# Kernel optimization log

Hardware: AMD Instinct MI355X
Metric: run time of the kernel (lower is better)

The kernel has to match this reference:

```python
import jax, jax.numpy as jnp
import numpy as np

N_NODES = 50000
N_EDGES = 500000
N_GRAPHS = 2000
HID = 145
N_CLS = 21
N_LAYERS = 4
EPS = 1e-5

def setup_inputs() -> dict:
    key = jax.random.key(0)
    ks = jax.random.split(key, 12)
    x = jax.random.randint(ks[0], (N_NODES,), 0, N_CLS)
    edge_index = jax.random.randint(ks[1], (2, N_EDGES), 0, N_NODES)
    batch_idx = jnp.sort(jax.random.randint(ks[2], (N_NODES,), 0, N_GRAPHS))
    s = 1.0 / np.sqrt(HID)
    emb = jax.random.normal(ks[3], (N_CLS, HID), jnp.float32)
    Wc = jax.random.uniform(ks[4], (N_LAYERS, HID, HID), jnp.float32, -s, s)
    bc = jax.random.uniform(ks[5], (N_LAYERS, HID), jnp.float32, -s, s)
    gamma = jnp.ones((N_LAYERS, HID), jnp.float32)
    beta = jnp.zeros((N_LAYERS, HID), jnp.float32)
    W1 = jax.random.uniform(ks[6], (HID, HID // 2), jnp.float32, -s, s)
    b1 = jax.random.uniform(ks[7], (HID // 2,), jnp.float32, -s, s)
    W2 = jax.random.uniform(ks[8], (HID // 2, 1), jnp.float32, -s, s)
    b2 = jax.random.uniform(ks[9], (1,), jnp.float32, -s, s)
    return {"x": x, "edge_index": edge_index, "batch_idx": batch_idx,
            "emb": emb, "Wc": Wc, "bc": bc, "gamma": gamma, "beta": beta,
            "W1": W1, "b1": b1, "W2": W2, "b2": b2}

def reference(x, edge_index, batch_idx, emb, Wc, bc, gamma, beta, W1, b1, W2, b2):
    N = x.shape[0]
    # gcn_norm with self loops: deg over targets (col), sym normalization
    loops = jnp.arange(N)
    row = jnp.concatenate([edge_index[0], loops])  # source
    col = jnp.concatenate([edge_index[1], loops])  # target
    deg = jax.ops.segment_sum(jnp.ones_like(row, jnp.float32), col, num_segments=N)
    dis = jnp.where(deg > 0, jax.lax.rsqrt(deg), 0.0)
    ew = dis[row] * dis[col]  # [E+N]

    h = emb[x]  # [N, HID]
    for l in range(N_LAYERS):
        h_in = h
        hw = h @ Wc[l]                                   # linear
        msg = hw[row] * ew[:, None]                      # gather + weight
        agg = jax.ops.segment_sum(msg, col, num_segments=N) + bc[l]  # scatter-add
        # BatchNorm1d (training-mode batch stats, biased var)
        mu = jnp.mean(agg, axis=0)
        var = jnp.mean((agg - mu) ** 2, axis=0)
        hbn = gamma[l] * (agg - mu) * jax.lax.rsqrt(var + EPS) + beta[l]
        h = jax.nn.relu(hbn) + h_in                      # relu + residual
    # global mean pool
    sums = jax.ops.segment_sum(h, batch_idx, num_segments=N_GRAPHS)
    cnt = jax.ops.segment_sum(jnp.ones((N,), jnp.float32), batch_idx, num_segments=N_GRAPHS)
    hg = sums / jnp.maximum(cnt, 1.0)[:, None]
    out = jax.nn.relu(hg @ W1 + b1) @ W2 + b2
    return out.reshape(-1, 1)
```

## Files before the change

### kernel.cpp

```cpp
#include <hip/hip_runtime.h>

#define N_NODES  50000
#define N_EDGES  500000
#define N_GRAPHS 2000
#define HID      145
#define HID2     72
#define N_LAYERS 4
#define EPS      1e-5f
#define HWS_LD   160
#define AGG_LD   152
#define BR       64
#define TSB      168
#define NBKT     64
#define GPSZ     (NBKT * 2 * AGG_LD)
#define NB_FILL  ((N_EDGES + 255) / 256)

typedef __attribute__((ext_vector_type(4))) float f32x4;
typedef __attribute__((ext_vector_type(2))) _Float16 f16x2;
typedef __attribute__((ext_vector_type(8))) _Float16 f16x8;

#define RFL(v) __builtin_amdgcn_readfirstlane(v)


__global__ void k_zero(int* __restrict__ hist, float* __restrict__ gpart) {
    int i = blockIdx.x * 256 + threadIdx.x;
    if (i < N_NODES) hist[i] = 0;
    if (i < N_LAYERS * GPSZ) gpart[i] = 0.f;
}


__global__ void k_hist(const int* __restrict__ col, int* __restrict__ hist) {
    int i = blockIdx.x * 256 + threadIdx.x;
    if (i < N_EDGES) atomicAdd(&hist[col[i]], 1);
}

__global__ void k_scan1(const int* __restrict__ cnt, int* __restrict__ incl,
                        int* __restrict__ part) {
    __shared__ int s[1024];
    int i = blockIdx.x * 1024 + threadIdx.x;
    int v = (i < N_NODES) ? cnt[i] : 0;
    s[threadIdx.x] = v;
    __syncthreads();
    for (int d = 1; d < 1024; d <<= 1) {
        int t = (threadIdx.x >= d) ? s[threadIdx.x - d] : 0;
        __syncthreads();
        s[threadIdx.x] += t;
        __syncthreads();
    }
    if (i < N_NODES) incl[i] = s[threadIdx.x];
    if (threadIdx.x == 1023) part[blockIdx.x] = s[1023];
}


__global__ void k_scan3(const int* __restrict__ incl, const int* __restrict__ cnt,
                        const int* __restrict__ part, int* __restrict__ starts,
                        int* __restrict__ cursor, float* __restrict__ dis) {
    __shared__ int sOff;
    int t = threadIdx.x;
    if (t < 64) {
        int v = (t < (int)blockIdx.x && t < 49) ? part[t] : 0;
#pragma unroll
        for (int d = 32; d > 0; d >>= 1) v += __shfl_xor(v, d);
        if (t == 0) sOff = v;
    }
    __syncthreads();
    int off = sOff;
    int i = blockIdx.x * 1024 + t;
    if (i < N_NODES) {
        int st = incl[i] - cnt[i] + off;
        starts[i] = st;
        cursor[i] = st;
        dis[i] = rsqrtf((float)(cnt[i] + 1));
    }
    if (i == 0) starts[N_NODES] = N_EDGES;
}


__global__ void k_fill_wfrag(const int* __restrict__ rowv, const int* __restrict__ colv,
                             int* __restrict__ cursor, int* __restrict__ csr,
                             const float* __restrict__ Wc, _Float16* __restrict__ Wfrag) {
    int b = blockIdx.x;
    if (b < NB_FILL) {
        int e = b * 256 + threadIdx.x;
        if (e < N_EDGES) {
            int c = colv[e];
            int p = atomicAdd(&cursor[c], 1);
            csr[p] = rowv[e];
        }
    } else {
        int fid = (b - NB_FILL) * 4 + (threadIdx.x >> 6);
        int l = threadIdx.x & 63;
        int layer = fid / 50, rem = fid - layer * 50;
        int kc = rem / 10, ct = rem - kc * 10;
        const float* Wl = Wc + (size_t)layer * HID * HID;
        _Float16* base = Wfrag + (size_t)fid * 512 + l * 8;
#pragma unroll
        for (int j = 0; j < 8; j++) {
            int k = kc * 32 + (l >> 4) * 8 + j;
            int c = ct * 16 + (l & 15);
            float v = (k < HID && c < HID) ? Wl[k * HID + c] : 0.f;
            base[j] = (_Float16)v;
        }
    }
}


#define MFMA16(a, b, c) __builtin_amdgcn_mfma_f32_16x16x32_f16(a, b, c, 0, 0, 0)

template <int MODE>
__global__ __launch_bounds__(512, 6) void k_gemm_fused(
    const _Float16* __restrict__ wfb, const float* __restrict__ dis,
    const int* __restrict__ x, const float* __restrict__ emb,
    const _Float16* __restrict__ agg, const float* __restrict__ gpart,
    const float* __restrict__ gamma, const float* __restrict__ beta,
    _Float16* __restrict__ h, _Float16* __restrict__ hws) {
    __shared__ _Float16 tile[BR * TSB];
    __shared__ float sA[HID], sB[HID];
    int t = threadIdx.x;
    int rbase = blockIdx.x * BR;
    if (MODE == 1 && t < HID) {
        float s_ = 0.f, q_ = 0.f;
        for (int b = 0; b < NBKT; b++) {
            s_ += gpart[b * (2 * AGG_LD) + t];
            q_ += gpart[b * (2 * AGG_LD) + AGG_LD + t];
        }
        const float inv = 1.f / (float)N_NODES;
        float mu = s_ * inv;
        float var = q_ * inv - mu * mu;
        float a = gamma[t] * rsqrtf(var + EPS);
        sA[t] = a;
        sB[t] = beta[t] - mu * a;
    }
    __syncthreads();
    for (int idx = t; idx < BR * 19; idx += 512) {
        int r = idx / 19;
        int c = idx - r * 19;
        int f0 = c * 8;
        int gr = rbase + r;
        f16x8 hst = {};
        if (gr < N_NODES) {
            size_t base = (size_t)gr * AGG_LD + f0;
            if (MODE == 0) {
                const float* er = emb + x[gr] * HID;
#pragma unroll
                for (int j = 0; j < 8; j++) {
                    int f = f0 + j;
                    hst[j] = (_Float16)((f < HID) ? er[f] : 0.f);
                }
            } else {
                f16x8 av = *(const f16x8*)(agg + base);
                f16x8 hv = *(const f16x8*)(h + base);
#pragma unroll
                for (int j = 0; j < 8; j++) {
                    int f = f0 + j;
                    float vj = 0.f;
                    if (f < HID) {
                        vj = fmaf(sA[f], (float)av[j], sB[f]);
                        vj = fmaxf(vj, 0.f) + (float)hv[j];
                    }
                    hst[j] = (_Float16)vj;
                }
            }
            *(f16x8*)(h + base) = hst;
        }
        *(f16x8*)&tile[r * TSB + f0] = hst;
    }
    if (t < BR) {
        f16x8 z = {};
        *(f16x8*)&tile[t * TSB + 152] = z;
    }
    __syncthreads();

    int w = t >> 6, l = t & 63;
    int rt = w & 3;
    int c5 = (w >> 2) * 5;
    int arow = rt * 16 + (l & 15);
    int kgrp = (l >> 4) * 8;
    f32x4 acc0 = {}, acc1 = {}, acc2 = {}, acc3 = {}, acc4 = {};
#pragma unroll
    for (int kc = 0; kc < 5; kc++) {
        f16x8 ah = *(const f16x8*)&tile[arow * TSB + kc * 32 + kgrp];
        const _Float16* p = wfb + (size_t)(kc * 10 + c5) * 512 + l * 8;
        f16x8 bh;
#define STEP(ACC, CI)                                                      \
        bh = *(const f16x8*)(p + (CI) * 512);                              \
        ACC = MFMA16(ah, bh, ACC);
        STEP(acc0, 0) STEP(acc1, 1) STEP(acc2, 2) STEP(acc3, 3) STEP(acc4, 4)
#undef STEP
    }
    int rb4 = rbase + rt * 16 + (l >> 4) * 4;
    f32x4 d4 = *(const f32x4*)(dis + rb4);
    int colb = c5 * 16 + (l & 15);
#pragma unroll
    for (int r_ = 0; r_ < 4; r_++) {
        int gr = rb4 + r_;
        if (gr < N_NODES) {
            float dd = d4[r_];
            _Float16* row = hws + (size_t)gr * HWS_LD + colb;
            row[0]  = (_Float16)(acc0[r_] * dd);
            row[16] = (_Float16)(acc1[r_] * dd);
            row[32] = (_Float16)(acc2[r_] * dd);
            row[48] = (_Float16)(acc3[r_] * dd);
            row[64] = (_Float16)(acc4[r_] * dd);
        }
    }
}


__global__ __launch_bounds__(256) void k_agg(const _Float16* __restrict__ hws,
                                             const int* __restrict__ starts,
                                             const int* __restrict__ csr,
                                             const float* __restrict__ dis,
                                             _Float16* __restrict__ agg,
                                             float* __restrict__ gpart) {
    __shared__ float sS[4][AGG_LD], sQ[4][AGG_LD];
    int t = threadIdx.x;
    int wave = t >> 6;
    int lane = t & 63;
    int i = RFL(blockIdx.x * 4 + wave);
    int s = RFL(starts[i]);
    int e = RFL(starts[i + 1]);
    bool tl = lane < 9;
    const f16x2* self = (const f16x2*)(hws + (size_t)i * HWS_LD);
    f16x2 sv = self[lane];
    float ax = (float)sv.x, ay = (float)sv.y;
    float bx = 0.f, by = 0.f;
    if (tl) { f16x2 tv = self[64 + lane]; bx = (float)tv.x; by = (float)tv.y; }
    int last = e - 1;
    for (int j = s; j < e; j += 8) {
        int rb[8]; float m[8];
#pragma unroll
        for (int u = 0; u < 8; u++) {
            int jj = j + u;
            bool ok = jj < e;
            rb[u] = RFL(csr[ok ? jj : last]) * HWS_LD;
            m[u] = ok ? 1.f : 0.f;
        }
#pragma unroll
        for (int u = 0; u < 8; u++) {
            f16x2 v = ((const f16x2*)(hws + rb[u]))[lane];
            ax = fmaf((float)v.x, m[u], ax);
            ay = fmaf((float)v.y, m[u], ay);
        }
        if (tl) {
#pragma unroll
            for (int u = 0; u < 8; u++) {
                f16x2 v = ((const f16x2*)(hws + rb[u]))[64 + lane];
                bx = fmaf((float)v.x, m[u], bx);
                by = fmaf((float)v.y, m[u], by);
            }
        }
    }
    float di = dis[i];
    float v0 = ax * di, v1 = ay * di;
    float v2 = bx * di;
    float v3 = (lane < 8) ? by * di : 0.f;

    f16x2* o2 = (f16x2*)(agg + (size_t)i * AGG_LD);
    o2[lane] = f16x2{(_Float16)v0, (_Float16)v1};
    if (tl) o2[64 + lane] = f16x2{(_Float16)v2, (_Float16)v3};

    sS[wave][2 * lane] = v0;     sQ[wave][2 * lane] = v0 * v0;
    sS[wave][2 * lane + 1] = v1; sQ[wave][2 * lane + 1] = v1 * v1;
    if (tl) {
        sS[wave][128 + 2 * lane] = v2; sQ[wave][128 + 2 * lane] = v2 * v2;
        sS[wave][129 + 2 * lane] = v3; sQ[wave][129 + 2 * lane] = v3 * v3;
    }
    __syncthreads();
    int bucket = blockIdx.x & (NBKT - 1);
    float* gp = gpart + (size_t)bucket * (2 * AGG_LD);
    for (int idx2 = t; idx2 < 2 * AGG_LD; idx2 += 256) {
        int f = (idx2 < AGG_LD) ? idx2 : idx2 - AGG_LD;
        if (f > HID) continue;
        float v = (idx2 < AGG_LD)
                      ? ((sS[0][f] + sS[1][f]) + (sS[2][f] + sS[3][f]))
                      : ((sQ[0][f] + sQ[1][f]) + (sQ[2][f] + sQ[3][f]));
        atomicAdd(&gp[idx2], v);
    }
}


__global__ __launch_bounds__(256) void k_bncoef(const float* __restrict__ gpart,
                                                const float* __restrict__ gamma,
                                                const float* __restrict__ beta,
                                                float* __restrict__ AB) {
    int w = blockIdx.x * 4 + (threadIdx.x >> 6);
    int lane = threadIdx.x & 63;
    if (w >= HID) return;
    const float* ps = gpart + (size_t)lane * (2 * AGG_LD) + w;
    float s = ps[0];
    float q = ps[AGG_LD];
#pragma unroll
    for (int d = 32; d > 0; d >>= 1) {
        s += __shfl_xor(s, d);
        q += __shfl_xor(q, d);
    }
    if (lane == 0) {
        const float inv = 1.f / (float)N_NODES;
        float mu = s * inv;
        float var = q * inv - mu * mu;
        float a = gamma[w] * rsqrtf(var + EPS);
        AB[w] = a;
        AB[HID + w] = beta[w] - mu * a;
    }
}


__global__ __launch_bounds__(192) void k_pool_mlp(
    const _Float16* __restrict__ agg, const _Float16* __restrict__ h,
    const float* __restrict__ AB, const int* __restrict__ batch,
    const float* __restrict__ W1, const float* __restrict__ b1,
    const float* __restrict__ W2, const float* __restrict__ b2,
    float* __restrict__ out) {
    __shared__ float sH[HID];
    __shared__ float red[128];
    int g = blockIdx.x;
    int lo = 0, hi = N_NODES;
    while (lo < hi) { int m = (lo + hi) >> 1; if (batch[m] < g) lo = m + 1; else hi = m; }
    int s = lo;
    hi = N_NODES;
    while (lo < hi) { int m = (lo + hi) >> 1; if (batch[m] < g + 1) lo = m + 1; else hi = m; }
    int e = lo;
    int f = threadIdx.x;
    if (f < HID) {
        float A = AB[f], B = AB[HID + f];
        float acc = 0.f;
        for (int n = s; n < e; n++) {
            size_t idx = (size_t)n * AGG_LD + f;
            float v = fmaf(A, (float)agg[idx], B);
            acc += fmaxf(v, 0.f) + (float)h[idx];
        }
        sH[f] = acc / fmaxf((float)(e - s), 1.f);
    }
    __syncthreads();
    int t = threadIdx.x;
    float v = 0.f;
    if (t < HID2) {
        float acc = b1[t];
        for (int k = 0; k < HID; k++) acc = fmaf(sH[k], W1[k * HID2 + t], acc);
        v = fmaxf(acc, 0.f) * W2[t];
    }
    if (t < 128) red[t] = v;
    __syncthreads();
    for (int d = 64; d > 0; d >>= 1) {
        if (t < d) red[t] += red[t + d];
        __syncthreads();
    }
    if (t == 0) out[g] = red[0] + b2[0];
}


extern "C" void kernel_launch(void* const* d_in, const int* in_sizes, int n_in,
                              void* d_out, int out_size, void* d_ws, size_t ws_size,
                              hipStream_t stream) {
    const int*   x     = (const int*)d_in[0];
    const int*   erow  = (const int*)d_in[1];
    const int*   ecol  = erow + N_EDGES;
    const int*   batch = (const int*)d_in[2];
    const float* emb   = (const float*)d_in[3];
    const float* Wc    = (const float*)d_in[4];
    const float* gamma = (const float*)d_in[6];
    const float* beta  = (const float*)d_in[7];
    const float* W1    = (const float*)d_in[8];
    const float* b1    = (const float*)d_in[9];
    const float* W2    = (const float*)d_in[10];
    const float* b2    = (const float*)d_in[11];
    float* out = (float*)d_out;

    char* wsb = (char*)d_ws;
    size_t off = 0;
    auto alloc = [&](size_t bytes) -> char* {
        char* p = wsb + off;
        off = (off + bytes + 255) & ~(size_t)255;
        return p;
    };
    int*      hist    = (int*)alloc(N_NODES * 4);
    int*      incl    = (int*)alloc(N_NODES * 4);
    int*      part    = (int*)alloc(64 * 4);
    int*      starts  = (int*)alloc((N_NODES + 1) * 4);
    int*      cursor  = (int*)alloc(N_NODES * 4);
    int*      csr     = (int*)alloc(N_EDGES * 4);
    float*    dis     = (float*)alloc((N_NODES + 64) * 4);
    _Float16* h       = (_Float16*)alloc((size_t)N_NODES * AGG_LD * 2);
    _Float16* hws     = (_Float16*)alloc((size_t)N_NODES * HWS_LD * 2);
    _Float16* agg     = (_Float16*)alloc((size_t)N_NODES * AGG_LD * 2);
    float*    gpart   = (float*)alloc((size_t)N_LAYERS * GPSZ * 4);
    float*    AB      = (float*)alloc(2 * HID * 4);
    _Float16* Wfrag   = (_Float16*)alloc((size_t)N_LAYERS * 50 * 512 * 2);

    const int NB_SCAN = (N_NODES + 1023) / 1024;
    const int NB_GEMM = (N_NODES + BR - 1) / BR;
    const int NB_ZERO = (N_LAYERS * GPSZ + 255) / 256;

    k_zero<<<(N_NODES > N_LAYERS * GPSZ ? (N_NODES + 255) / 256 : NB_ZERO), 256, 0, stream>>>(hist, gpart);
    k_hist<<<(N_EDGES + 255) / 256, 256, 0, stream>>>(ecol, hist);
    k_scan1<<<NB_SCAN, 1024, 0, stream>>>(hist, incl, part);
    k_scan3<<<NB_SCAN, 1024, 0, stream>>>(incl, hist, part, starts, cursor, dis);
    k_fill_wfrag<<<NB_FILL + 50, 256, 0, stream>>>(erow, ecol, cursor, csr, Wc, Wfrag);

    for (int l = 0; l < N_LAYERS; l++) {
        const _Float16* wfb = Wfrag + (size_t)l * 50 * 512;
        if (l == 0)
            k_gemm_fused<0><<<NB_GEMM, 512, 0, stream>>>(
                wfb, dis, x, emb, agg, nullptr, nullptr, nullptr, h, hws);
        else
            k_gemm_fused<1><<<NB_GEMM, 512, 0, stream>>>(
                wfb, dis, x, emb, agg, gpart + (size_t)(l - 1) * GPSZ,
                gamma + (l - 1) * HID, beta + (l - 1) * HID, h, hws);
        k_agg<<<N_NODES / 4, 256, 0, stream>>>(hws, starts, csr, dis, agg,
                                               gpart + (size_t)l * GPSZ);
    }

    k_bncoef<<<(HID + 3) / 4, 256, 0, stream>>>(gpart + (size_t)3 * GPSZ,
                                                gamma + 3 * HID, beta + 3 * HID, AB);
    k_pool_mlp<<<N_GRAPHS, 192, 0, stream>>>(agg, h, AB, batch, W1, b1, W2, b2, out);
}
```

Measured before the change: 381.6 us.

## Merge scan kernels, fold BN coef into pool, split agg loop, halve buckets

Merges the two-pass prefix scan into one kernel in which each block recomputes its own offset by summing the preceding counts. The final-layer BN coefficient kernel is folded into the pooling kernel, so every block recomputes the coefficients from the bucket partials. The aggregation loop gets a mask-free main loop over full groups of eight edges and a masked tail, and the number of stats buckets drops from 64 to 32. The intent is fewer kernel launches and less work in the inner loop, at the cost of redundant reads in the scan and pool kernels and more atomic contention per bucket.

```diff
diff --git a/kernel.cpp b/kernel.cpp
--- a/kernel.cpp
+++ b/kernel.cpp
@@ -11,7 +11,7 @@
 #define AGG_LD   152
 #define BR       64
 #define TSB      168
-#define NBKT     64
+#define NBKT     32
 #define GPSZ     (NBKT * 2 * AGG_LD)
 #define NB_FILL  ((N_EDGES + 255) / 256)
 
@@ -34,43 +34,39 @@
     if (i < N_EDGES) atomicAdd(&hist[col[i]], 1);
 }
 
-__global__ void k_scan1(const int* __restrict__ cnt, int* __restrict__ incl,
-                        int* __restrict__ part) {
+
+__global__ void k_scan(const int* __restrict__ cnt, int* __restrict__ starts,
+                       int* __restrict__ cursor, float* __restrict__ dis) {
     __shared__ int s[1024];
-    int i = blockIdx.x * 1024 + threadIdx.x;
+    __shared__ int sOff;
+    int b = blockIdx.x, t = threadIdx.x;
+    int i = b * 1024 + t;
     int v = (i < N_NODES) ? cnt[i] : 0;
-    s[threadIdx.x] = v;
+    int pre = 0;
+    for (int k = t; k < b * 1024; k += 1024) pre += cnt[k];
+    s[t] = pre;
+    __syncthreads();
+    for (int d = 512; d > 0; d >>= 1) {
+        if (t < d) s[t] += s[t + d];
+        __syncthreads();
+    }
+    if (t == 0) sOff = s[0];
+    __syncthreads();
+    int off = sOff;
+    __syncthreads();
+    s[t] = v;
     __syncthreads();
     for (int d = 1; d < 1024; d <<= 1) {
-        int t = (threadIdx.x >= d) ? s[threadIdx.x - d] : 0;
+        int x = (t >= d) ? s[t - d] : 0;
         __syncthreads();
-        s[threadIdx.x] += t;
+        s[t] += x;
         __syncthreads();
     }
-    if (i < N_NODES) incl[i] = s[threadIdx.x];
-    if (threadIdx.x == 1023) part[blockIdx.x] = s[1023];
-}
-
-
-__global__ void k_scan3(const int* __restrict__ incl, const int* __restrict__ cnt,
-                        const int* __restrict__ part, int* __restrict__ starts,
-                        int* __restrict__ cursor, float* __restrict__ dis) {
-    __shared__ int sOff;
-    int t = threadIdx.x;
-    if (t < 64) {
-        int v = (t < (int)blockIdx.x && t < 49) ? part[t] : 0;
-#pragma unroll
-        for (int d = 32; d > 0; d >>= 1) v += __shfl_xor(v, d);
-        if (t == 0) sOff = v;
-    }
-    __syncthreads();
-    int off = sOff;
-    int i = blockIdx.x * 1024 + t;
     if (i < N_NODES) {
-        int st = incl[i] - cnt[i] + off;
+        int st = off + s[t] - v;
         starts[i] = st;
         cursor[i] = st;
-        dis[i] = rsqrtf((float)(cnt[i] + 1));
+        dis[i] = rsqrtf((float)(v + 1));
     }
     if (i == 0) starts[N_NODES] = N_EDGES;
 }
@@ -226,14 +222,36 @@
     float ax = (float)sv.x, ay = (float)sv.y;
     float bx = 0.f, by = 0.f;
     if (tl) { f16x2 tv = self[64 + lane]; bx = (float)tv.x; by = (float)tv.y; }
-    int last = e - 1;
-    for (int j = s; j < e; j += 8) {
+
+    int nfull = (e - s) & ~7;
+    int efull = s + nfull;
+    int j = s;
+    for (; j < efull; j += 8) {
+        int rb[8];
+#pragma unroll
+        for (int u = 0; u < 8; u++) rb[u] = RFL(csr[j + u]) * HWS_LD;
+#pragma unroll
+        for (int u = 0; u < 8; u++) {
+            f16x2 v = ((const f16x2*)(hws + rb[u]))[lane];
+            ax += (float)v.x;
+            ay += (float)v.y;
+        }
+        if (tl) {
+#pragma unroll
+            for (int u = 0; u < 8; u++) {
+                f16x2 v = ((const f16x2*)(hws + rb[u]))[64 + lane];
+                bx += (float)v.x;
+                by += (float)v.y;
+            }
+        }
+    }
+    if (j < e) {
+        int last = e - 1;
         int rb[8]; float m[8];
 #pragma unroll
         for (int u = 0; u < 8; u++) {
-            int jj = j + u;
-            bool ok = jj < e;
-            rb[u] = RFL(csr[ok ? jj : last]) * HWS_LD;
+            bool ok = j + u < e;
+            rb[u] = RFL(csr[ok ? j + u : last]) * HWS_LD;
             m[u] = ok ? 1.f : 0.f;
         }
 #pragma unroll
@@ -251,6 +269,7 @@
             }
         }
     }
+
     float di = dis[i];
     float v0 = ax * di, v1 = ay * di;
     float v2 = bx * di;
@@ -280,40 +299,31 @@
 }
 
 
-__global__ __launch_bounds__(256) void k_bncoef(const float* __restrict__ gpart,
-                                                const float* __restrict__ gamma,
-                                                const float* __restrict__ beta,
-                                                float* __restrict__ AB) {
-    int w = blockIdx.x * 4 + (threadIdx.x >> 6);
-    int lane = threadIdx.x & 63;
-    if (w >= HID) return;
-    const float* ps = gpart + (size_t)lane * (2 * AGG_LD) + w;
-    float s = ps[0];
-    float q = ps[AGG_LD];
-#pragma unroll
-    for (int d = 32; d > 0; d >>= 1) {
-        s += __shfl_xor(s, d);
-        q += __shfl_xor(q, d);
-    }
-    if (lane == 0) {
-        const float inv = 1.f / (float)N_NODES;
-        float mu = s * inv;
-        float var = q * inv - mu * mu;
-        float a = gamma[w] * rsqrtf(var + EPS);
-        AB[w] = a;
-        AB[HID + w] = beta[w] - mu * a;
-    }
-}
-
-
 __global__ __launch_bounds__(192) void k_pool_mlp(
     const _Float16* __restrict__ agg, const _Float16* __restrict__ h,
-    const float* __restrict__ AB, const int* __restrict__ batch,
+    const float* __restrict__ gpart, const float* __restrict__ gamma,
+    const float* __restrict__ beta, const int* __restrict__ batch,
     const float* __restrict__ W1, const float* __restrict__ b1,
     const float* __restrict__ W2, const float* __restrict__ b2,
     float* __restrict__ out) {
+    __shared__ float sA[HID], sB[HID];
     __shared__ float sH[HID];
     __shared__ float red[128];
+    int f = threadIdx.x;
+    if (f < HID) {
+        float s_ = 0.f, q_ = 0.f;
+        for (int b = 0; b < NBKT; b++) {
+            s_ += gpart[b * (2 * AGG_LD) + f];
+            q_ += gpart[b * (2 * AGG_LD) + AGG_LD + f];
+        }
+        const float inv = 1.f / (float)N_NODES;
+        float mu = s_ * inv;
+        float var = q_ * inv - mu * mu;
+        float a = gamma[f] * rsqrtf(var + EPS);
+        sA[f] = a;
+        sB[f] = beta[f] - mu * a;
+    }
+    __syncthreads();
     int g = blockIdx.x;
     int lo = 0, hi = N_NODES;
     while (lo < hi) { int m = (lo + hi) >> 1; if (batch[m] < g) lo = m + 1; else hi = m; }
@@ -321,9 +331,8 @@
     hi = N_NODES;
     while (lo < hi) { int m = (lo + hi) >> 1; if (batch[m] < g + 1) lo = m + 1; else hi = m; }
     int e = lo;
-    int f = threadIdx.x;
     if (f < HID) {
-        float A = AB[f], B = AB[HID + f];
+        float A = sA[f], B = sB[f];
         float acc = 0.f;
         for (int n = s; n < e; n++) {
             size_t idx = (size_t)n * AGG_LD + f;
@@ -375,8 +384,6 @@
         return p;
     };
     int*      hist    = (int*)alloc(N_NODES * 4);
-    int*      incl    = (int*)alloc(N_NODES * 4);
-    int*      part    = (int*)alloc(64 * 4);
     int*      starts  = (int*)alloc((N_NODES + 1) * 4);
     int*      cursor  = (int*)alloc(N_NODES * 4);
     int*      csr     = (int*)alloc(N_EDGES * 4);
@@ -385,17 +392,14 @@
     _Float16* hws     = (_Float16*)alloc((size_t)N_NODES * HWS_LD * 2);
     _Float16* agg     = (_Float16*)alloc((size_t)N_NODES * AGG_LD * 2);
     float*    gpart   = (float*)alloc((size_t)N_LAYERS * GPSZ * 4);
-    float*    AB      = (float*)alloc(2 * HID * 4);
     _Float16* Wfrag   = (_Float16*)alloc((size_t)N_LAYERS * 50 * 512 * 2);
 
     const int NB_SCAN = (N_NODES + 1023) / 1024;
     const int NB_GEMM = (N_NODES + BR - 1) / BR;
-    const int NB_ZERO = (N_LAYERS * GPSZ + 255) / 256;
-
-    k_zero<<<(N_NODES > N_LAYERS * GPSZ ? (N_NODES + 255) / 256 : NB_ZERO), 256, 0, stream>>>(hist, gpart);
+
+    k_zero<<<(N_NODES + 255) / 256, 256, 0, stream>>>(hist, gpart);
     k_hist<<<(N_EDGES + 255) / 256, 256, 0, stream>>>(ecol, hist);
-    k_scan1<<<NB_SCAN, 1024, 0, stream>>>(hist, incl, part);
-    k_scan3<<<NB_SCAN, 1024, 0, stream>>>(incl, hist, part, starts, cursor, dis);
+    k_scan<<<NB_SCAN, 1024, 0, stream>>>(hist, starts, cursor, dis);
     k_fill_wfrag<<<NB_FILL + 50, 256, 0, stream>>>(erow, ecol, cursor, csr, Wc, Wfrag);
 
     for (int l = 0; l < N_LAYERS; l++) {
@@ -411,7 +415,7 @@
                                                gpart + (size_t)l * GPSZ);
     }
 
-    k_bncoef<<<(HID + 3) / 4, 256, 0, stream>>>(gpart + (size_t)3 * GPSZ,
-                                                gamma + 3 * HID, beta + 3 * HID, AB);
-    k_pool_mlp<<<N_GRAPHS, 192, 0, stream>>>(agg, h, AB, batch, W1, b1, W2, b2, out);
-}
+    k_pool_mlp<<<N_GRAPHS, 192, 0, stream>>>(agg, h, gpart + (size_t)3 * GPSZ,
+                                             gamma + 3 * HID, beta + 3 * HID,
+                                             batch, W1, b1, W2, b2, out);
+}
```

After: 385.8 us. Within noise of the previous version (+1.1%).
